# Kernel optimization log

Hardware: AMD Instinct MI355X
Metric: run time of the kernel (lower is better)

## Reference

```python
import jax, jax.numpy as jnp
import numpy as np

IN_DIM, HID, OUT_DIM = 2048, 2560, 2048
KERNEL = 4  # causal depthwise temporal conv width (Griffin uses 4)
C_RGLRU = 8.0  # Griffin's fixed scalar c in a_t = a^(c*r_t)


def setup_inputs() -> dict:
    key = jax.random.key(0)
    ks = jax.random.split(key, 16)
    s = 0.02
    return {
        "x": jax.random.normal(ks[0], (4, 2048, IN_DIM), jnp.float32),
        "Wl": jax.random.normal(ks[1], (IN_DIM, HID), jnp.float32) * s,
        "bl": jnp.zeros((HID,), jnp.float32),
        "Wr": jax.random.normal(ks[2], (IN_DIM, HID), jnp.float32) * s,
        "br": jnp.zeros((HID,), jnp.float32),
        "conv_w": jax.random.normal(ks[3], (KERNEL, 1, HID), jnp.float32) * 0.1,
        "conv_b": jnp.zeros((HID,), jnp.float32),
        "Wa": jax.random.normal(ks[4], (HID, HID), jnp.float32) * s,
        "ba": jnp.zeros((HID,), jnp.float32),
        "Wi": jax.random.normal(ks[5], (HID, HID), jnp.float32) * s,
        "bi": jnp.zeros((HID,), jnp.float32),
        "lam": jax.random.normal(ks[6], (HID,), jnp.float32) + 2.0,  # Lambda; sigmoid(lam)~0.88 decay
        "Wo": jax.random.normal(ks[7], (HID, OUT_DIM), jnp.float32) * s,
        "bo": jnp.zeros((OUT_DIM,), jnp.float32),
    }


def _rg_lru(u, Wa, ba, Wi, bi, lam):
    # u: [B,S,H]. a_t = exp(c * r_t * log sigmoid(lam)); log sigmoid = -softplus(-lam)
    r = jax.nn.sigmoid(jnp.einsum("bsh,hk->bsk", u, Wa) + ba)
    i = jax.nn.sigmoid(jnp.einsum("bsh,hk->bsk", u, Wi) + bi)
    log_a = (-C_RGLRU * jax.nn.softplus(-lam)) * r          # [B,S,H], <= 0
    a = jnp.exp(log_a)
    beta = jnp.sqrt(jnp.maximum(1.0 - jnp.exp(2.0 * log_a), 1e-12))
    drive = beta * (i * u)                                   # [B,S,H]

    def step(h, ab):
        a_t, d_t = ab
        h = a_t * h + d_t
        return h, h

    h0 = jnp.zeros((u.shape[0], u.shape[2]), u.dtype)
    _, hs = jax.lax.scan(step, h0, (a.transpose(1, 0, 2), drive.transpose(1, 0, 2)))
    return hs.transpose(1, 0, 2)  # [B,S,H]


def reference(x, Wl, bl, Wr, br, conv_w, conv_b, Wa, ba, Wi, bi, lam, Wo, bo):
    # left (GLU) branch
    left = jax.nn.gelu(jnp.einsum("bsd,dh->bsh", x, Wl) + bl)
    # right branch: linear -> causal depthwise conv1d -> RG-LRU
    r_in = jnp.einsum("bsd,dh->bsh", x, Wr) + br             # [B,S,H]
    conv = jax.lax.conv_general_dilated(
        r_in, conv_w, window_strides=(1,), padding=[(KERNEL - 1, 0)],
        dimension_numbers=("NWC", "WIO", "NWC"), feature_group_count=HID,
    ) + conv_b
    right = _rg_lru(conv, Wa, ba, Wi, bi, lam)
    return jnp.einsum("bsh,ho->bso", left * right, Wo) + bo
```

## Files before the change

kernel.cpp:

```cpp
#include <hip/hip_runtime.h>
#include <stdint.h>

#define B_ 4
#define S_ 2048
#define D_ 2048
#define H_ 2560
#define O_ 2048
#define M_ (B_*S_)
#define NCH 16
#define LCH (S_/NCH)

typedef __attribute__((ext_vector_type(8))) short bf16x8;
typedef __attribute__((ext_vector_type(4))) float f32x4;

typedef const __attribute__((address_space(1))) unsigned int* gp32;
typedef __attribute__((address_space(3))) unsigned int* lp32;

__device__ __forceinline__ void async_cp16(const unsigned short* g, unsigned short* l) {
    __builtin_amdgcn_global_load_lds((gp32)g, (lp32)l, 16, 0, 0);
}

__device__ __forceinline__ unsigned short f2bf(float f) {
    unsigned int x = __float_as_uint(f);
    x += 0x7fffu + ((x >> 16) & 1u);
    return (unsigned short)(x >> 16);
}
__device__ __forceinline__ float bf2f(unsigned short s) {
    return __uint_as_float(((unsigned int)s) << 16);
}
__device__ __forceinline__ float4 ld_bf4(const unsigned short* p) {
    const uint2 u = *(const uint2*)p;
    float4 r;
    r.x = bf2f((unsigned short)(u.x & 0xffffu));
    r.y = bf2f((unsigned short)(u.x >> 16));
    r.z = bf2f((unsigned short)(u.y & 0xffffu));
    r.w = bf2f((unsigned short)(u.y >> 16));
    return r;
}
__device__ __forceinline__ float fast_sigmoid(float x) { return 1.0f / (1.0f + __expf(-x)); }
__device__ __forceinline__ float gelu_tanh(float x) {
    float t = 0.7978845608028654f * (x + 0.044715f * x * x * x);
    float e = __expf(2.0f * t);
    float th = 1.0f - 2.0f / (e + 1.0f);
    return 0.5f * x * (1.0f + th);
}

__global__ void cast_x_kernel(const float* __restrict__ in, unsigned short* __restrict__ out, int n4) {
    int gid = blockIdx.x * 256 + threadIdx.x;
    if (gid >= n4) return;
    const float4 v = ((const float4*)in)[gid];
    union { unsigned short s[4]; uint2 u; } pk;
    pk.s[0] = f2bf(v.x); pk.s[1] = f2bf(v.y); pk.s[2] = f2bf(v.z); pk.s[3] = f2bf(v.w);
    ((uint2*)out)[gid] = pk.u;
}

__global__ void transpose_cast_kernel(const float* __restrict__ in, unsigned short* __restrict__ out,
                                      int K, int N) {
    __shared__ float tile[64][65];
    const int t = threadIdx.x;
    const int k0 = blockIdx.y * 64, n0 = blockIdx.x * 64;
    const int r = t >> 4, c4 = (t & 15) * 4;
    #pragma unroll
    for (int p = 0; p < 4; ++p) {
        const float4 v = *(const float4*)(in + (size_t)(k0 + p*16 + r) * N + n0 + c4);
        tile[p*16 + r][c4+0] = v.x;
        tile[p*16 + r][c4+1] = v.y;
        tile[p*16 + r][c4+2] = v.z;
        tile[p*16 + r][c4+3] = v.w;
    }
    __syncthreads();
    #pragma unroll
    for (int p = 0; p < 4; ++p) {
        const int nn = n0 + p*16 + r;
        union { unsigned short s[4]; uint2 u; } pk;
        #pragma unroll
        for (int j = 0; j < 4; ++j) pk.s[j] = f2bf(tile[c4 + j][p*16 + r]);
        *(uint2*)(out + (size_t)nn * K + k0 + c4) = pk.u;
    }
}

template <int MODE>
__global__ __launch_bounds__(256, 4) void gemm_kernel(
        const unsigned short* __restrict__ A,
        const unsigned short* __restrict__ Bt,
        const int K,
        const float* __restrict__ bias0,
        const float* __restrict__ bias1,
        void* __restrict__ out0,
        void* __restrict__ out1)
{
    __shared__ __align__(16) unsigned short As[128*64];
    __shared__ __align__(16) unsigned short Bs[128*64];
    const int t = threadIdx.x;
    const int m0 = blockIdx.y * 128;
    const int n0 = blockIdx.x * 128;

    const int srow = t >> 3;
    const int csrc = ((t & 7) ^ (srow & 7)) * 8;
    const unsigned short* gA = A  + (size_t)(m0 + srow) * K + csrc;
    const unsigned short* gB = Bt + (size_t)(n0 + srow) * K + csrc;
    unsigned short* lA = As + t * 8;
    unsigned short* lB = Bs + t * 8;
    const size_t gstep = (size_t)32 * K;

    const int lane = t & 63;
    const int w = t >> 6;
    const int wm = (w >> 1) * 64;
    const int wn = (w & 1) * 64;
    const int q = lane >> 4;
    const int l16 = lane & 15;

    f32x4 acc[4][4];
    #pragma unroll
    for (int i = 0; i < 4; ++i)
        #pragma unroll
        for (int j = 0; j < 4; ++j)
            acc[i][j] = (f32x4){0.f, 0.f, 0.f, 0.f};

    for (int k0 = 0; k0 < K; k0 += 64) {
        #pragma unroll
        for (int j = 0; j < 4; ++j) {
            async_cp16(gA + j * gstep, lA + j * 2048);
            async_cp16(gB + j * gstep, lB + j * 2048);
        }
        gA += 64; gB += 64;
        __syncthreads();
        #pragma unroll
        for (int ks = 0; ks < 2; ++ks) {
            const int ch = ((q + ks * 4) ^ (l16 & 7)) * 8;
            bf16x8 af[4], bfr[4];
            #pragma unroll
            for (int f = 0; f < 4; ++f)
                af[f]  = *(const bf16x8*)(As + (wm + f*16 + l16) * 64 + ch);
            #pragma unroll
            for (int f = 0; f < 4; ++f)
                bfr[f] = *(const bf16x8*)(Bs + (wn + f*16 + l16) * 64 + ch);
            #pragma unroll
            for (int fm = 0; fm < 4; ++fm)
                #pragma unroll
                for (int fn = 0; fn < 4; ++fn)
                    acc[fm][fn] = __builtin_amdgcn_mfma_f32_16x16x32_bf16(af[fm], bfr[fn], acc[fm][fn], 0, 0, 0);
        }
        __syncthreads();
    }

    const int rbase = q * 4;
    #pragma unroll
    for (int fm = 0; fm < 4; ++fm) {
        #pragma unroll
        for (int fn = 0; fn < 4; ++fn) {
            const int cc = n0 + wn + fn * 16 + l16;
            #pragma unroll
            for (int j = 0; j < 4; ++j) {
                const int rr = m0 + wm + fm * 16 + rbase + j;
                float v = acc[fm][fn][j];
                if (MODE == 0) {
                    if (cc < H_) {
                        ((unsigned short*)out0)[(size_t)rr * H_ + cc] = f2bf(gelu_tanh(v + bias0[cc]));
                    } else {
                        const int c2 = cc - H_;
                        ((unsigned short*)out1)[(size_t)rr * H_ + c2] = f2bf(v + bias1[c2]);
                    }
                } else if (MODE == 1) {
                    if (cc < H_) {
                        ((unsigned short*)out0)[(size_t)rr * H_ + cc] = f2bf(fast_sigmoid(v + bias0[cc]));
                    } else {
                        const int c2 = cc - H_;
                        ((unsigned short*)out1)[(size_t)rr * H_ + c2] = f2bf(fast_sigmoid(v + bias1[c2]));
                    }
                } else {
                    ((float*)out0)[(size_t)rr * O_ + cc] = v + bias0[cc];
                }
            }
        }
    }
}

__global__ void conv_kernel(const unsigned short* __restrict__ rin,
                            const float* __restrict__ cw,
                            const float* __restrict__ cb,
                            unsigned short* __restrict__ ub)
{
    const int gid = blockIdx.x * 256 + threadIdx.x;
    const int h = (gid % (H_/4)) * 4;
    const int tmp = gid / (H_/4);
    const int s0 = (tmp % (S_/4)) * 4;
    const int b = tmp / (S_/4);
    const unsigned short* base = rin + (size_t)b * S_ * H_ + h;
    float4 rows[7];
    #pragma unroll
    for (int idx = 0; idx < 7; ++idx) {
        const int s = s0 - 3 + idx;
        if (s >= 0) rows[idx] = ld_bf4(base + (size_t)s * H_);
        else        rows[idx] = make_float4(0.f, 0.f, 0.f, 0.f);
    }
    float4 w[4];
    #pragma unroll
    for (int j = 0; j < 4; ++j) w[j] = *(const float4*)(cw + j * H_ + h);
    const float4 bias = *(const float4*)(cb + h);
    #pragma unroll
    for (int p = 0; p < 4; ++p) {
        float ox = bias.x, oy = bias.y, oz = bias.z, ow = bias.w;
        #pragma unroll
        for (int j = 0; j < 4; ++j) {
            ox += w[j].x * rows[p + j].x;
            oy += w[j].y * rows[p + j].y;
            oz += w[j].z * rows[p + j].z;
            ow += w[j].w * rows[p + j].w;
        }
        const size_t oidx = (size_t)b * S_ * H_ + (size_t)(s0 + p) * H_ + h;
        union { unsigned short s4[4]; uint2 uu; } pk;
        pk.s4[0] = f2bf(ox); pk.s4[1] = f2bf(oy); pk.s4[2] = f2bf(oz); pk.s4[3] = f2bf(ow);
        *(uint2*)(ub + oidx) = pk.uu;
    }
}

__global__ void scan_pass1(const unsigned short* __restrict__ rg,
                           const unsigned short* __restrict__ ig,
                           const unsigned short* __restrict__ ub,
                           const float* __restrict__ lam,
                           float* __restrict__ Asum,
                           float* __restrict__ Hend)
{
    const int tid = blockIdx.x * 256 + threadIdx.x;
    const int h = tid % H_;
    const int t2 = tid / H_;
    const int c = t2 % NCH;
    const int b = t2 / NCH;
    const float kh = -8.0f * log1pf(__expf(-lam[h]));
    size_t idx = ((size_t)b * S_ + (size_t)c * LCH) * H_ + h;
    float A = 1.f, hs = 0.f;
    #pragma unroll 4
    for (int s = 0; s < LCH; ++s, idx += H_) {
        const float rv = bf2f(rg[idx]);
        const float iv = bf2f(ig[idx]);
        const float uv = bf2f(ub[idx]);
        const float a = __expf(kh * rv);
        const float beta = sqrtf(fmaxf(1.f - a * a, 1e-12f));
        hs = a * hs + beta * iv * uv;
        A *= a;
    }
    Asum[tid] = A;
    Hend[tid] = hs;
}

__global__ void scan_pass2(const float* __restrict__ Asum, float* __restrict__ Hend) {
    const int tid = blockIdx.x * 256 + threadIdx.x;
    const int h = tid % H_;
    const int b = tid / H_;
    float hin = 0.f;
    #pragma unroll
    for (int c = 0; c < NCH; ++c) {
        const int q = (b * NCH + c) * H_ + h;
        const float Ac = Asum[q];
        const float he = Hend[q];
        Hend[q] = hin;
        hin = he + Ac * hin;
    }
}

__global__ void scan_pass3(const unsigned short* __restrict__ rg,
                           const unsigned short* __restrict__ ig,
                           const unsigned short* __restrict__ ub,
                           const unsigned short* __restrict__ leftb,
                           const float* __restrict__ lam,
                           const float* __restrict__ Hin,
                           unsigned short* __restrict__ lrb)
{
    const int tid = blockIdx.x * 256 + threadIdx.x;
    const int h = tid % H_;
    const int t2 = tid / H_;
    const int c = t2 % NCH;
    const int b = t2 / NCH;
    const float kh = -8.0f * log1pf(__expf(-lam[h]));
    size_t idx = ((size_t)b * S_ + (size_t)c * LCH) * H_ + h;
    float hs = Hin[tid];
    #pragma unroll 4
    for (int s = 0; s < LCH; ++s, idx += H_) {
        const float rv = bf2f(rg[idx]);
        const float iv = bf2f(ig[idx]);
        const float uv = bf2f(ub[idx]);
        const float lf = bf2f(leftb[idx]);
        const float a = __expf(kh * rv);
        const float beta = sqrtf(fmaxf(1.f - a * a, 1e-12f));
        hs = a * hs + beta * iv * uv;
        lrb[idx] = f2bf(lf * hs);
    }
}

extern "C" void kernel_launch(void* const* d_in, const int* in_sizes, int n_in,
                              void* d_out, int out_size, void* d_ws, size_t ws_size,
                              hipStream_t stream)
{
    const float* x   = (const float*)d_in[0];
    const float* Wl  = (const float*)d_in[1];
    const float* bl  = (const float*)d_in[2];
    const float* Wr  = (const float*)d_in[3];
    const float* br  = (const float*)d_in[4];
    const float* cw  = (const float*)d_in[5];
    const float* cb  = (const float*)d_in[6];
    const float* Wa  = (const float*)d_in[7];
    const float* ba  = (const float*)d_in[8];
    const float* Wi  = (const float*)d_in[9];
    const float* bi  = (const float*)d_in[10];
    const float* lam = (const float*)d_in[11];
    const float* Wo  = (const float*)d_in[12];
    const float* bo  = (const float*)d_in[13];
    float* out = (float*)d_out;
    (void)in_sizes; (void)n_in; (void)out_size;

    const size_t wWlr = (size_t)2 * H_ * D_ * 2;
    const size_t wWai = (size_t)2 * H_ * H_ * 2;
    const size_t wWo  = (size_t)O_ * H_ * 2;
    auto al = [](size_t b) { return (b + 255) & ~(size_t)255; };

    int nchunk = 4;
    for (int n = 1; n <= 4; n *= 2) {
        const size_t Mc = M_ / n;
        const size_t Bc = Mc / S_;
        const size_t need = al(wWlr) + al(wWai) + al(wWo)
                          + 4 * al(Mc * H_ * 2)
                          + 2 * al(Bc * NCH * H_ * 4);
        if (need <= ws_size) { nchunk = n; break; }
    }
    const int Mc = M_ / nchunk;
    const int Bc = Mc / S_;
    const size_t actB = (size_t)Mc * H_ * 2;

    char* p = (char*)d_ws;
    size_t off = 0;
    auto alloc = [&](size_t bytes) -> void* {
        void* q = p + off;
        off += al(bytes);
        return q;
    };
    unsigned short* WlrT  = (unsigned short*)alloc(wWlr);
    unsigned short* WaiT  = (unsigned short*)alloc(wWai);
    unsigned short* WoT   = (unsigned short*)alloc(wWo);
    unsigned short* slotX = (unsigned short*)alloc(actB);
    unsigned short* slotL = (unsigned short*)alloc(actB);
    unsigned short* slotR = (unsigned short*)alloc(actB);
    unsigned short* slotU = (unsigned short*)alloc(actB);
    float* Asum = (float*)alloc((size_t)Bc * NCH * H_ * 4);
    float* Hend = (float*)alloc((size_t)Bc * NCH * H_ * 4);

    transpose_cast_kernel<<<dim3(H_/64, D_/64), dim3(256), 0, stream>>>(Wl, WlrT, D_, H_);
    transpose_cast_kernel<<<dim3(H_/64, D_/64), dim3(256), 0, stream>>>(Wr, WlrT + (size_t)H_*D_, D_, H_);
    transpose_cast_kernel<<<dim3(H_/64, H_/64), dim3(256), 0, stream>>>(Wa, WaiT, H_, H_);
    transpose_cast_kernel<<<dim3(H_/64, H_/64), dim3(256), 0, stream>>>(Wi, WaiT + (size_t)H_*H_, H_, H_);
    transpose_cast_kernel<<<dim3(O_/64, H_/64), dim3(256), 0, stream>>>(Wo, WoT, H_, O_);

    for (int c = 0; c < nchunk; ++c) {
        const float* xc = x + (size_t)c * Mc * D_;
        float* outc = out + (size_t)c * Mc * O_;
        unsigned short* xb    = slotX;
        unsigned short* leftb = slotL;
        unsigned short* rinb  = slotR;
        unsigned short* ub    = slotU;
        unsigned short* rgb   = slotX;
        unsigned short* igb   = slotR;
        unsigned short* lrb   = slotX;

        cast_x_kernel<<<dim3(Mc*D_/4/256), dim3(256), 0, stream>>>(xc, xb, Mc*D_/4);
        gemm_kernel<0><<<dim3((2*H_)/128, Mc/128), dim3(256), 0, stream>>>(xb, WlrT, D_, bl, br, leftb, rinb);
        conv_kernel<<<dim3(Bc*S_*H_/16/256), dim3(256), 0, stream>>>(rinb, cw, cb, ub);
        gemm_kernel<1><<<dim3((2*H_)/128, Mc/128), dim3(256), 0, stream>>>(ub, WaiT, H_, ba, bi, rgb, igb);
        scan_pass1<<<dim3(Bc*NCH*H_/256), dim3(256), 0, stream>>>(rgb, igb, ub, lam, Asum, Hend);
        scan_pass2<<<dim3(Bc*H_/256), dim3(256), 0, stream>>>(Asum, Hend);
        scan_pass3<<<dim3(Bc*NCH*H_/256), dim3(256), 0, stream>>>(rgb, igb, ub, leftb, lam, Hend, lrb);
        gemm_kernel<2><<<dim3(O_/128, Mc/128), dim3(256), 0, stream>>>(lrb, WoT, H_, bo, nullptr, outc, nullptr);
    }
}
```

Baseline: 811.2 us.

## Rewrite GEMM as 256x256 double-buffered ping-pong pipeline with grid swizzle

Replaces the single-buffered 128x128 GEMM with a 256x256 tile, 512-thread kernel that double-buffers A and B in LDS, issues async global-to-LDS loads for the next k-tile between quarter-steps of MFMA work, and uses explicit barriers, waitcnt and setprio to interleave loads with compute. It also remaps block indices with an XCD-style swizzle to improve L2 locality, and restructures the epilogue so left/right branch selection is per-block. This aims to hide global load latency and raise arithmetic intensity, at the cost of 128KB of LDS per block, more registers, and fragile hand-tuned synchronisation.

Result: slower. 848.8 us (+4.6%).

```diff
diff --git a/kernel.cpp b/kernel.cpp
--- a/kernel.cpp
+++ b/kernel.cpp
@@ -79,8 +79,106 @@
     }
 }
 
+#define GEMM_TILE(ASC, BSC, BSN, TT)                                           \
+  do {                                                                         \
+    const int kb_b = ((TT) + 1 < nt) ? ((TT) + 1) * 64 : 0;                    \
+    const int kb_a = ((TT) + 2 < nt) ? ((TT) + 2) * 64 : 0;                    \
+                \
+    _Pragma("unroll")                                                          \
+    for (int f = 0; f < 4; ++f) {                                              \
+      a0[f][0] = *(const bf16x8*)(ASC + rbaseA + f * 1024 + ch0);              \
+      a0[f][1] = *(const bf16x8*)(ASC + rbaseA + f * 1024 + ch1);              \
+    }                                                                          \
+    _Pragma("unroll")                                                          \
+    for (int f = 0; f < 2; ++f) {                                              \
+      b0[f][0] = *(const bf16x8*)(BSC + rbaseB + f * 1024 + ch0);              \
+      b0[f][1] = *(const bf16x8*)(BSC + rbaseB + f * 1024 + ch1);              \
+    }                                                                          \
+    async_cp16(gB + kb_b,          BSN + ldst);                                \
+    async_cp16(gB + kb_b + gr64,   BSN + ldst + 4096);                         \
+    __builtin_amdgcn_s_barrier();                                              \
+    asm volatile("s_waitcnt lgkmcnt(0)" ::: "memory");                         \
+    __builtin_amdgcn_sched_barrier(0);                                         \
+    __builtin_amdgcn_s_setprio(1);                                             \
+    _Pragma("unroll")                                                          \
+    for (int ks = 0; ks < 2; ++ks)                                             \
+      _Pragma("unroll")                                                        \
+      for (int f = 0; f < 4; ++f)                                              \
+        _Pragma("unroll")                                                      \
+        for (int g = 0; g < 2; ++g)                                            \
+          acc[f][g] = __builtin_amdgcn_mfma_f32_16x16x32_bf16(                 \
+              a0[f][ks], b0[g][ks], acc[f][g], 0, 0, 0);                       \
+    __builtin_amdgcn_s_setprio(0);                                             \
+    __builtin_amdgcn_s_barrier();                                              \
+    __builtin_amdgcn_sched_barrier(0);                                         \
+                   \
+    _Pragma("unroll")                                                          \
+    for (int f = 0; f < 4; ++f) {                                              \
+      a1[f][0] = *(const bf16x8*)(ASC + rbaseA + 4096 + f * 1024 + ch0);       \
+      a1[f][1] = *(const bf16x8*)(ASC + rbaseA + 4096 + f * 1024 + ch1);       \
+    }                                                                          \
+    async_cp16(gB + kb_b + 2 * gr64, BSN + 8192 + ldst);                       \
+    async_cp16(gB + kb_b + 3 * gr64, BSN + 8192 + ldst + 4096);                \
+    __builtin_amdgcn_s_barrier();                                              \
+    asm volatile("s_waitcnt lgkmcnt(0)" ::: "memory");                         \
+    __builtin_amdgcn_sched_barrier(0);                                         \
+    __builtin_amdgcn_s_setprio(1);                                             \
+    _Pragma("unroll")                                                          \
+    for (int ks = 0; ks < 2; ++ks)                                             \
+      _Pragma("unroll")                                                        \
+      for (int f = 0; f < 4; ++f)                                              \
+        _Pragma("unroll")                                                      \
+        for (int g = 0; g < 2; ++g)                                            \
+          acc[4 + f][g] = __builtin_amdgcn_mfma_f32_16x16x32_bf16(             \
+              a1[f][ks], b0[g][ks], acc[4 + f][g], 0, 0, 0);                   \
+    __builtin_amdgcn_s_setprio(0);                                             \
+    __builtin_amdgcn_s_barrier();                                              \
+    __builtin_amdgcn_sched_barrier(0);                                         \
+                   \
+    _Pragma("unroll")                                                          \
+    for (int f = 0; f < 2; ++f) {                                              \
+      b1[f][0] = *(const bf16x8*)(BSC + rbaseB + 2048 + f * 1024 + ch0);       \
+      b1[f][1] = *(const bf16x8*)(BSC + rbaseB + 2048 + f * 1024 + ch1);       \
+    }                                                                          \
+    async_cp16(gA + kb_a,        ASC + ldst);                                  \
+    async_cp16(gA + kb_a + gr64, ASC + ldst + 4096);                           \
+    __builtin_amdgcn_s_barrier();                                              \
+    asm volatile("s_waitcnt lgkmcnt(0)" ::: "memory");                         \
+    __builtin_amdgcn_sched_barrier(0);                                         \
+    __builtin_amdgcn_s_setprio(1);                                             \
+    _Pragma("unroll")                                                          \
+    for (int ks = 0; ks < 2; ++ks)                                             \
+      _Pragma("unroll")                                                        \
+      for (int f = 0; f < 4; ++f)                                              \
+        _Pragma("unroll")                                                      \
+        for (int g = 0; g < 2; ++g)                                            \
+          acc[f][2 + g] = __builtin_amdgcn_mfma_f32_16x16x32_bf16(             \
+              a0[f][ks], b1[g][ks], acc[f][2 + g], 0, 0, 0);                   \
+    __builtin_amdgcn_s_setprio(0);                                             \
+    __builtin_amdgcn_s_barrier();                                              \
+    __builtin_amdgcn_sched_barrier(0);                                         \
+                  \
+    async_cp16(gA + kb_a + 2 * gr64, ASC + 8192 + ldst);                       \
+    async_cp16(gA + kb_a + 3 * gr64, ASC + 8192 + ldst + 4096);                \
+    asm volatile("s_waitcnt vmcnt(4)" ::: "memory");                           \
+    __builtin_amdgcn_sched_barrier(0);                                         \
+    __builtin_amdgcn_s_barrier();                                              \
+    __builtin_amdgcn_s_setprio(1);                                             \
+    _Pragma("unroll")                                                          \
+    for (int ks = 0; ks < 2; ++ks)                                             \
+      _Pragma("unroll")                                                        \
+      for (int f = 0; f < 4; ++f)                                              \
+        _Pragma("unroll")                                                      \
+        for (int g = 0; g < 2; ++g)                                            \
+          acc[4 + f][2 + g] = __builtin_amdgcn_mfma_f32_16x16x32_bf16(         \
+              a1[f][ks], b1[g][ks], acc[4 + f][2 + g], 0, 0, 0);               \
+    __builtin_amdgcn_s_setprio(0);                                             \
+    __builtin_amdgcn_s_barrier();                                              \
+    __builtin_amdgcn_sched_barrier(0);                                         \
+  } while (0)
+
 template <int MODE>
-__global__ __launch_bounds__(256, 4) void gemm_kernel(
+__global__ __launch_bounds__(512, 2) void gemm_kernel(
         const unsigned short* __restrict__ A,
         const unsigned short* __restrict__ Bt,
         const int K,
@@ -89,87 +187,105 @@
         void* __restrict__ out0,
         void* __restrict__ out1)
 {
-    __shared__ __align__(16) unsigned short As[128*64];
-    __shared__ __align__(16) unsigned short Bs[128*64];
+    __shared__ __align__(16) unsigned short As0[256*64];
+    __shared__ __align__(16) unsigned short As1[256*64];
+    __shared__ __align__(16) unsigned short Bs0[256*64];
+    __shared__ __align__(16) unsigned short Bs1[256*64];
+
     const int t = threadIdx.x;
-    const int m0 = blockIdx.y * 128;
-    const int n0 = blockIdx.x * 128;
+
+    const int nx = gridDim.x;
+    const int nwg = gridDim.x * gridDim.y;
+    int lin = blockIdx.y * nx + blockIdx.x;
+    lin = (lin & 7) * (nwg >> 3) + (lin >> 3);
+    const int m0 = (lin / nx) * 256;
+    const int n0 = (lin % nx) * 256;
 
     const int srow = t >> 3;
-    const int csrc = ((t & 7) ^ (srow & 7)) * 8;
-    const unsigned short* gA = A  + (size_t)(m0 + srow) * K + csrc;
-    const unsigned short* gB = Bt + (size_t)(n0 + srow) * K + csrc;
-    unsigned short* lA = As + t * 8;
-    unsigned short* lB = Bs + t * 8;
-    const size_t gstep = (size_t)32 * K;
+    const int scol = ((t & 7) ^ (srow & 7)) * 8;
+    const unsigned short* gA = A  + (size_t)(m0 + srow) * K + scol;
+    const unsigned short* gB = Bt + (size_t)(n0 + srow) * K + scol;
+    const size_t gr64 = (size_t)64 * K;
+    const int ldst = t * 8;
 
     const int lane = t & 63;
     const int w = t >> 6;
-    const int wm = (w >> 1) * 64;
-    const int wn = (w & 1) * 64;
+    const int wm = w >> 2;
+    const int wn = w & 3;
     const int q = lane >> 4;
     const int l16 = lane & 15;
 
-    f32x4 acc[4][4];
-    #pragma unroll
-    for (int i = 0; i < 4; ++i)
+    const int rbaseA = (wm * 128 + l16) * 64;
+    const int rbaseB = (wn * 64 + l16) * 64;
+    const int ch0 = ((q)     ^ (l16 & 7)) * 8;
+    const int ch1 = ((q + 4) ^ (l16 & 7)) * 8;
+
+    const int nt = K >> 6;
+
+    f32x4 acc[8][4];
+    #pragma unroll
+    for (int i = 0; i < 8; ++i)
         #pragma unroll
         for (int j = 0; j < 4; ++j)
             acc[i][j] = (f32x4){0.f, 0.f, 0.f, 0.f};
 
-    for (int k0 = 0; k0 < K; k0 += 64) {
+    bf16x8 a0[4][2], a1[4][2], b0[2][2], b1[2][2];
+
+    async_cp16(gA,            As0 + ldst);
+    async_cp16(gA + gr64,     As0 + ldst + 4096);
+    async_cp16(gA + 2*gr64,   As0 + 8192 + ldst);
+    async_cp16(gA + 3*gr64,   As0 + 8192 + ldst + 4096);
+    async_cp16(gB,            Bs0 + ldst);
+    async_cp16(gB + gr64,     Bs0 + ldst + 4096);
+    async_cp16(gB + 2*gr64,   Bs0 + 8192 + ldst);
+    async_cp16(gB + 3*gr64,   Bs0 + 8192 + ldst + 4096);
+    async_cp16(gA + 64,           As1 + ldst);
+    async_cp16(gA + 64 + gr64,    As1 + ldst + 4096);
+    async_cp16(gA + 64 + 2*gr64,  As1 + 8192 + ldst);
+    async_cp16(gA + 64 + 3*gr64,  As1 + 8192 + ldst + 4096);
+    asm volatile("s_waitcnt vmcnt(4)" ::: "memory");
+    __builtin_amdgcn_sched_barrier(0);
+    __builtin_amdgcn_s_barrier();
+
+    for (int tt = 0; tt < nt; tt += 2) {
+        GEMM_TILE(As0, Bs0, Bs1, tt);
+        GEMM_TILE(As1, Bs1, Bs0, tt + 1);
+    }
+    asm volatile("s_waitcnt vmcnt(0)" ::: "memory");
+
+    const int rb = q * 4;
+    if (MODE == 2) {
+        float* op = (float*)out0;
         #pragma unroll
-        for (int j = 0; j < 4; ++j) {
-            async_cp16(gA + j * gstep, lA + j * 2048);
-            async_cp16(gB + j * gstep, lB + j * 2048);
-        }
-        gA += 64; gB += 64;
-        __syncthreads();
-        #pragma unroll
-        for (int ks = 0; ks < 2; ++ks) {
-            const int ch = ((q + ks * 4) ^ (l16 & 7)) * 8;
-            bf16x8 af[4], bfr[4];
-            #pragma unroll
-            for (int f = 0; f < 4; ++f)
-                af[f]  = *(const bf16x8*)(As + (wm + f*16 + l16) * 64 + ch);
-            #pragma unroll
-            for (int f = 0; f < 4; ++f)
-                bfr[f] = *(const bf16x8*)(Bs + (wn + f*16 + l16) * 64 + ch);
-            #pragma unroll
-            for (int fm = 0; fm < 4; ++fm)
-                #pragma unroll
-                for (int fn = 0; fn < 4; ++fn)
-                    acc[fm][fn] = __builtin_amdgcn_mfma_f32_16x16x32_bf16(af[fm], bfr[fn], acc[fm][fn], 0, 0, 0);
-        }
-        __syncthreads();
-    }
-
-    const int rbase = q * 4;
-    #pragma unroll
-    for (int fm = 0; fm < 4; ++fm) {
-        #pragma unroll
-        for (int fn = 0; fn < 4; ++fn) {
-            const int cc = n0 + wn + fn * 16 + l16;
+        for (int i = 0; i < 8; ++i) {
+            const int rr = m0 + wm * 128 + (i >> 2) * 64 + (i & 3) * 16 + rb;
             #pragma unroll
             for (int j = 0; j < 4; ++j) {
-                const int rr = m0 + wm + fm * 16 + rbase + j;
-                float v = acc[fm][fn][j];
-                if (MODE == 0) {
-                    if (cc < H_) {
-                        ((unsigned short*)out0)[(size_t)rr * H_ + cc] = f2bf(gelu_tanh(v + bias0[cc]));
-                    } else {
-                        const int c2 = cc - H_;
-                        ((unsigned short*)out1)[(size_t)rr * H_ + c2] = f2bf(v + bias1[c2]);
-                    }
-                } else if (MODE == 1) {
-                    if (cc < H_) {
-                        ((unsigned short*)out0)[(size_t)rr * H_ + cc] = f2bf(fast_sigmoid(v + bias0[cc]));
-                    } else {
-                        const int c2 = cc - H_;
-                        ((unsigned short*)out1)[(size_t)rr * H_ + c2] = f2bf(fast_sigmoid(v + bias1[c2]));
-                    }
-                } else {
-                    ((float*)out0)[(size_t)rr * O_ + cc] = v + bias0[cc];
+                const int cc = n0 + wn * 64 + (j >> 1) * 32 + (j & 1) * 16 + l16;
+                const float bb = bias0[cc];
+                #pragma unroll
+                for (int jj = 0; jj < 4; ++jj)
+                    op[(size_t)(rr + jj) * O_ + cc] = acc[i][j][jj] + bb;
+            }
+        }
+    } else {
+        const bool left = (n0 < H_);
+        const float* bias = left ? bias0 : bias1;
+        unsigned short* op = (unsigned short*)(left ? out0 : out1);
+        const int nb = left ? n0 : (n0 - H_);
+        #pragma unroll
+        for (int i = 0; i < 8; ++i) {
+            const int rr = m0 + wm * 128 + (i >> 2) * 64 + (i & 3) * 16 + rb;
+            #pragma unroll
+            for (int j = 0; j < 4; ++j) {
+                const int cc = nb + wn * 64 + (j >> 1) * 32 + (j & 1) * 16 + l16;
+                const float bb = bias[cc];
+                #pragma unroll
+                for (int jj = 0; jj < 4; ++jj) {
+                    float v = acc[i][j][jj] + bb;
+                    if (MODE == 0) v = left ? gelu_tanh(v) : v;
+                    else           v = fast_sigmoid(v);
+                    op[(size_t)(rr + jj) * H_ + cc] = f2bf(v);
                 }
             }
         }
@@ -362,12 +478,12 @@
         unsigned short* lrb   = slotX;
 
         cast_x_kernel<<<dim3(Mc*D_/4/256), dim3(256), 0, stream>>>(xc, xb, Mc*D_/4);
-        gemm_kernel<0><<<dim3((2*H_)/128, Mc/128), dim3(256), 0, stream>>>(xb, WlrT, D_, bl, br, leftb, rinb);
+        gemm_kernel<0><<<dim3((2*H_)/256, Mc/256), dim3(512), 0, stream>>>(xb, WlrT, D_, bl, br, leftb, rinb);
         conv_kernel<<<dim3(Bc*S_*H_/16/256), dim3(256), 0, stream>>>(rinb, cw, cb, ub);
-        gemm_kernel<1><<<dim3((2*H_)/128, Mc/128), dim3(256), 0, stream>>>(ub, WaiT, H_, ba, bi, rgb, igb);
+        gemm_kernel<1><<<dim3((2*H_)/256, Mc/256), dim3(512), 0, stream>>>(ub, WaiT, H_, ba, bi, rgb, igb);
         scan_pass1<<<dim3(Bc*NCH*H_/256), dim3(256), 0, stream>>>(rgb, igb, ub, lam, Asum, Hend);
         scan_pass2<<<dim3(Bc*H_/256), dim3(256), 0, stream>>>(Asum, Hend);
         scan_pass3<<<dim3(Bc*NCH*H_/256), dim3(256), 0, stream>>>(rgb, igb, ub, leftb, lam, Hend, lrb);
-        gemm_kernel<2><<<dim3(O_/128, Mc/128), dim3(256), 0, stream>>>(lrb, WoT, H_, bo, nullptr, outc, nullptr);
-    }
-}
+        gemm_kernel<2><<<dim3(O_/256, Mc/256), dim3(512), 0, stream>>>(lrb, WoT, H_, bo, nullptr, outc, nullptr);
+    }
+}
```

## Use 256x256-tile ping-pong pipelined GEMM for output projection

Applied to the files above, without the earlier changes.

Replaces the 128x128 output-projection GEMM with a new 512-thread kernel using 256x256 tiles, double-buffered LDS with async global-to-LDS copies, interleaved partial-tile MFMA phases with priority hints, and a grouped block-index remap for L2 locality. The aim is more data reuse per loaded tile and overlap of loads with MFMA work. It uses 128KB of LDS per block and a large accumulator set, which constrains occupancy, and the grid of 8x(Mc/256) blocks may underfill the device for small chunks.

New measurement: 835.2 us. 1.03x slower.

```diff
diff --git a/kernel.cpp b/kernel.cpp
--- a/kernel.cpp
+++ b/kernel.cpp
@@ -172,6 +172,149 @@
                     ((float*)out0)[(size_t)rr * O_ + cc] = v + bias0[cc];
                 }
             }
+        }
+    }
+}
+
+#define LDA2(dst, base)                                                        \
+    _Pragma("unroll")                                                          \
+    for (int f = 0; f < 4; ++f) {                                              \
+      dst[f][0] = *(const bf16x8*)((base) + rbaseA + f * 1024 + ch0);          \
+      dst[f][1] = *(const bf16x8*)((base) + rbaseA + f * 1024 + ch1);          \
+    }
+#define LDB2(dst, base)                                                        \
+    _Pragma("unroll")                                                          \
+    for (int f = 0; f < 2; ++f) {                                              \
+      dst[f][0] = *(const bf16x8*)((base) + rbaseB + f * 1024 + ch0);          \
+      dst[f][1] = *(const bf16x8*)((base) + rbaseB + f * 1024 + ch1);          \
+    }
+#define MM2(ar, br, i0, j0)                                                    \
+    __builtin_amdgcn_s_setprio(1);                                             \
+    _Pragma("unroll")                                                          \
+    for (int ks = 0; ks < 2; ++ks)                                             \
+      _Pragma("unroll")                                                        \
+      for (int f = 0; f < 4; ++f)                                              \
+        _Pragma("unroll")                                                      \
+        for (int g = 0; g < 2; ++g)                                            \
+          acc[(i0) + f][(j0) + g] = __builtin_amdgcn_mfma_f32_16x16x32_bf16(   \
+              ar[f][ks], br[g][ks], acc[(i0) + f][(j0) + g], 0, 0, 0);         \
+    __builtin_amdgcn_s_setprio(0);
+#define STG2(gptr, kk, lbuf, half)                                             \
+    async_cp16((gptr) + (size_t)(kk) + (size_t)((half)*2)   * gr64,            \
+               (lbuf) + (half)*8192 + ldst);                                   \
+    async_cp16((gptr) + (size_t)(kk) + (size_t)((half)*2+1) * gr64,            \
+               (lbuf) + (half)*8192 + ldst + 4096);
+#define BAR2() __builtin_amdgcn_s_barrier()
+
+__global__ __launch_bounds__(512, 2) void gemm256_k2(
+        const unsigned short* __restrict__ A,
+        const unsigned short* __restrict__ Bt,
+        const int K,
+        const float* __restrict__ bias0,
+        float* __restrict__ out0)
+{
+    __shared__ __align__(16) unsigned short As0[256*64];
+    __shared__ __align__(16) unsigned short As1[256*64];
+    __shared__ __align__(16) unsigned short Bs0[256*64];
+    __shared__ __align__(16) unsigned short Bs1[256*64];
+
+    const int t = threadIdx.x;
+
+    const int nx = gridDim.x;
+    const int nwg = gridDim.x * gridDim.y;
+    int lin = blockIdx.y * nx + blockIdx.x;
+    lin = (lin & 7) * (nwg >> 3) + (lin >> 3);
+    const int m0 = (lin / nx) * 256;
+    const int n0 = (lin % nx) * 256;
+
+    const int srow = t >> 3;
+    const int scol = ((t & 7) ^ (srow & 7)) * 8;
+    const unsigned short* gA = A  + (size_t)(m0 + srow) * K + scol;
+    const unsigned short* gB = Bt + (size_t)(n0 + srow) * K + scol;
+    const size_t gr64 = (size_t)64 * K;
+    const int ldst = t * 8;
+
+    const int lane = t & 63;
+    const int w = t >> 6;
+    const int wm = w >> 2;
+    const int wn = w & 3;
+    const int q = lane >> 4;
+    const int l16 = lane & 15;
+
+    const int rbaseA = (wm * 128 + l16) * 64;
+    const int rbaseB = (wn * 64 + l16) * 64;
+    const int ch0 = ((q)     ^ (l16 & 7)) * 8;
+    const int ch1 = ((q + 4) ^ (l16 & 7)) * 8;
+
+    const int nt = K >> 6;
+
+    f32x4 acc[8][4];
+    #pragma unroll
+    for (int i = 0; i < 8; ++i)
+        #pragma unroll
+        for (int j = 0; j < 4; ++j)
+            acc[i][j] = (f32x4){0.f, 0.f, 0.f, 0.f};
+
+    bf16x8 a0[4][2], a1[4][2], b0[2][2], b1[2][2];
+
+    STG2(gA, 0, As0, 0); STG2(gA, 0, As0, 1);
+    STG2(gB, 0, Bs0, 0); STG2(gB, 0, Bs0, 1);
+    STG2(gA, 64, As1, 0); STG2(gA, 64, As1, 1);
+    asm volatile("s_waitcnt vmcnt(4)" ::: "memory");
+    BAR2();
+
+    for (int tt = 0; tt < nt; tt += 2) {
+        const size_t kb1 = (size_t)((tt + 1 < nt) ? (tt + 1) * 64 : 0);
+        const size_t ka2 = (size_t)((tt + 2 < nt) ? (tt + 2) * 64 : 0);
+        const size_t kb2 = ka2;
+        const size_t ka3 = (size_t)((tt + 3 < nt) ? (tt + 3) * 64 : 0);
+
+        LDA2(a0, As0); LDB2(b0, Bs0);
+        STG2(gB, kb1, Bs1, 0);
+        MM2(a0, b0, 0, 0);
+        BAR2();
+        LDA2(a1, As0 + 4096);
+        STG2(gB, kb1, Bs1, 1);
+        MM2(a1, b0, 4, 0);
+        BAR2();
+        LDB2(b1, Bs0 + 2048);
+        STG2(gA, ka2, As0, 0);
+        MM2(a0, b1, 0, 2);
+        BAR2();
+        STG2(gA, ka2, As0, 1);
+        MM2(a1, b1, 4, 2);
+        asm volatile("s_waitcnt vmcnt(4)" ::: "memory");
+        BAR2();
+        LDA2(a0, As1); LDB2(b0, Bs1);
+        STG2(gB, kb2, Bs0, 0);
+        MM2(a0, b0, 0, 0);
+        BAR2();
+        LDA2(a1, As1 + 4096);
+        STG2(gB, kb2, Bs0, 1);
+        MM2(a1, b0, 4, 0);
+        BAR2();
+        LDB2(b1, Bs1 + 2048);
+        STG2(gA, ka3, As1, 0);
+        MM2(a0, b1, 0, 2);
+        BAR2();
+        STG2(gA, ka3, As1, 1);
+        MM2(a1, b1, 4, 2);
+        asm volatile("s_waitcnt vmcnt(4)" ::: "memory");
+        BAR2();
+    }
+    asm volatile("s_waitcnt vmcnt(0)" ::: "memory");
+
+    const int rb = q * 4;
+    #pragma unroll
+    for (int i = 0; i < 8; ++i) {
+        const int rr = m0 + wm * 128 + (i >> 2) * 64 + (i & 3) * 16 + rb;
+        #pragma unroll
+        for (int j = 0; j < 4; ++j) {
+            const int cc = n0 + wn * 64 + (j >> 1) * 32 + (j & 1) * 16 + l16;
+            const float bb = bias0[cc];
+            #pragma unroll
+            for (int jj = 0; jj < 4; ++jj)
+                out0[(size_t)(rr + jj) * O_ + cc] = acc[i][j][jj] + bb;
         }
     }
 }
@@ -368,6 +511,6 @@
         scan_pass1<<<dim3(Bc*NCH*H_/256), dim3(256), 0, stream>>>(rgb, igb, ub, lam, Asum, Hend);
         scan_pass2<<<dim3(Bc*H_/256), dim3(256), 0, stream>>>(Asum, Hend);
         scan_pass3<<<dim3(Bc*NCH*H_/256), dim3(256), 0, stream>>>(rgb, igb, ub, leftb, lam, Hend, lrb);
-        gemm_kernel<2><<<dim3(O_/128, Mc/128), dim3(256), 0, stream>>>(lrb, WoT, H_, bo, nullptr, outc, nullptr);
-    }
-}
+        gemm256_k2<<<dim3(O_/256, Mc/256), dim3(512), 0, stream>>>(lrb, WoT, H_, bo, outc);
+    }
+}
```

## Vectorize scan passes to 4 channels per thread, raise chunk count, merge weight transposes

Applied to the files above, without the earlier changes.

Each scan thread now handles four adjacent hidden channels, using 8-byte bf16 loads and stores instead of 2-byte scalar accesses. The sequence chunk count rises from 16 to 64, which keeps the number of scan threads up while shortening each serial chunk. The five weight transpose-cast launches become one launch with a z-dimension selecting the matrix. The goal is better memory coalescing and fewer launches, at the cost of more partial-sum traffic and a longer serial pass2.

Measured after the change: 850.2 us, median of 2. +4.8%, slower.

```diff
diff --git a/kernel.cpp b/kernel.cpp
--- a/kernel.cpp
+++ b/kernel.cpp
@@ -7,7 +7,7 @@
 #define H_ 2560
 #define O_ 2048
 #define M_ (B_*S_)
-#define NCH 16
+#define NCH 64
 #define LCH (S_/NCH)
 
 typedef __attribute__((ext_vector_type(8))) short bf16x8;
@@ -37,6 +37,11 @@
     r.w = bf2f((unsigned short)(u.y >> 16));
     return r;
 }
+__device__ __forceinline__ uint2 st_bf4(float a, float b, float c, float d) {
+    union { unsigned short s[4]; uint2 u; } pk;
+    pk.s[0] = f2bf(a); pk.s[1] = f2bf(b); pk.s[2] = f2bf(c); pk.s[3] = f2bf(d);
+    return pk.u;
+}
 __device__ __forceinline__ float fast_sigmoid(float x) { return 1.0f / (1.0f + __expf(-x)); }
 __device__ __forceinline__ float gelu_tanh(float x) {
     float t = 0.7978845608028654f * (x + 0.044715f * x * x * x);
@@ -49,20 +54,31 @@
     int gid = blockIdx.x * 256 + threadIdx.x;
     if (gid >= n4) return;
     const float4 v = ((const float4*)in)[gid];
-    union { unsigned short s[4]; uint2 u; } pk;
-    pk.s[0] = f2bf(v.x); pk.s[1] = f2bf(v.y); pk.s[2] = f2bf(v.z); pk.s[3] = f2bf(v.w);
-    ((uint2*)out)[gid] = pk.u;
-}
-
-__global__ void transpose_cast_kernel(const float* __restrict__ in, unsigned short* __restrict__ out,
-                                      int K, int N) {
+    ((uint2*)out)[gid] = st_bf4(v.x, v.y, v.z, v.w);
+}
+
+__global__ void transpose_all_kernel(const float* __restrict__ Wl, const float* __restrict__ Wr,
+                                     const float* __restrict__ Wa, const float* __restrict__ Wi,
+                                     const float* __restrict__ Wo,
+                                     unsigned short* __restrict__ WlrT,
+                                     unsigned short* __restrict__ WaiT,
+                                     unsigned short* __restrict__ WoT) {
     __shared__ float tile[64][65];
+    const float* src; unsigned short* dst; int K, N;
+    switch (blockIdx.z) {
+        case 0:  src = Wl; dst = WlrT;                       K = D_; N = H_; break;
+        case 1:  src = Wr; dst = WlrT + (size_t)H_ * D_;     K = D_; N = H_; break;
+        case 2:  src = Wa; dst = WaiT;                       K = H_; N = H_; break;
+        case 3:  src = Wi; dst = WaiT + (size_t)H_ * H_;     K = H_; N = H_; break;
+        default: src = Wo; dst = WoT;                        K = H_; N = O_; break;
+    }
+    const int k0 = blockIdx.y * 64, n0 = blockIdx.x * 64;
+    if (k0 >= K || n0 >= N) return;
     const int t = threadIdx.x;
-    const int k0 = blockIdx.y * 64, n0 = blockIdx.x * 64;
     const int r = t >> 4, c4 = (t & 15) * 4;
     #pragma unroll
     for (int p = 0; p < 4; ++p) {
-        const float4 v = *(const float4*)(in + (size_t)(k0 + p*16 + r) * N + n0 + c4);
+        const float4 v = *(const float4*)(src + (size_t)(k0 + p*16 + r) * N + n0 + c4);
         tile[p*16 + r][c4+0] = v.x;
         tile[p*16 + r][c4+1] = v.y;
         tile[p*16 + r][c4+2] = v.z;
@@ -72,10 +88,9 @@
     #pragma unroll
     for (int p = 0; p < 4; ++p) {
         const int nn = n0 + p*16 + r;
-        union { unsigned short s[4]; uint2 u; } pk;
-        #pragma unroll
-        for (int j = 0; j < 4; ++j) pk.s[j] = f2bf(tile[c4 + j][p*16 + r]);
-        *(uint2*)(out + (size_t)nn * K + k0 + c4) = pk.u;
+        *(uint2*)(dst + (size_t)nn * K + k0 + c4) =
+            st_bf4(tile[c4+0][p*16 + r], tile[c4+1][p*16 + r],
+                   tile[c4+2][p*16 + r], tile[c4+3][p*16 + r]);
     }
 }
 
@@ -209,9 +224,7 @@
             ow += w[j].w * rows[p + j].w;
         }
         const size_t oidx = (size_t)b * S_ * H_ + (size_t)(s0 + p) * H_ + h;
-        union { unsigned short s4[4]; uint2 uu; } pk;
-        pk.s4[0] = f2bf(ox); pk.s4[1] = f2bf(oy); pk.s4[2] = f2bf(oz); pk.s4[3] = f2bf(ow);
-        *(uint2*)(ub + oidx) = pk.uu;
+        *(uint2*)(ub + oidx) = st_bf4(ox, oy, oz, ow);
     }
 }
 
@@ -223,39 +236,56 @@
                            float* __restrict__ Hend)
 {
     const int tid = blockIdx.x * 256 + threadIdx.x;
-    const int h = tid % H_;
-    const int t2 = tid / H_;
+    const int h4 = (tid % (H_/4)) * 4;
+    const int t2 = tid / (H_/4);
     const int c = t2 % NCH;
     const int b = t2 / NCH;
-    const float kh = -8.0f * log1pf(__expf(-lam[h]));
-    size_t idx = ((size_t)b * S_ + (size_t)c * LCH) * H_ + h;
-    float A = 1.f, hs = 0.f;
+    const float4 lm = *(const float4*)(lam + h4);
+    float kh[4];
+    kh[0] = -8.0f * log1pf(__expf(-lm.x));
+    kh[1] = -8.0f * log1pf(__expf(-lm.y));
+    kh[2] = -8.0f * log1pf(__expf(-lm.z));
+    kh[3] = -8.0f * log1pf(__expf(-lm.w));
+    size_t idx = ((size_t)b * S_ + (size_t)c * LCH) * H_ + h4;
+    float A[4] = {1.f, 1.f, 1.f, 1.f};
+    float hs[4] = {0.f, 0.f, 0.f, 0.f};
     #pragma unroll 4
     for (int s = 0; s < LCH; ++s, idx += H_) {
-        const float rv = bf2f(rg[idx]);
-        const float iv = bf2f(ig[idx]);
-        const float uv = bf2f(ub[idx]);
-        const float a = __expf(kh * rv);
-        const float beta = sqrtf(fmaxf(1.f - a * a, 1e-12f));
-        hs = a * hs + beta * iv * uv;
-        A *= a;
-    }
-    Asum[tid] = A;
-    Hend[tid] = hs;
-}
-
-__global__ void scan_pass2(const float* __restrict__ Asum, float* __restrict__ Hend) {
+        const float4 rv = ld_bf4(rg + idx);
+        const float4 iv = ld_bf4(ig + idx);
+        const float4 uv = ld_bf4(ub + idx);
+        const float rr[4] = {rv.x, rv.y, rv.z, rv.w};
+        const float ii[4] = {iv.x, iv.y, iv.z, iv.w};
+        const float uu[4] = {uv.x, uv.y, uv.z, uv.w};
+        #pragma unroll
+        for (int j = 0; j < 4; ++j) {
+            const float a = __expf(kh[j] * rr[j]);
+            const float beta = sqrtf(fmaxf(1.f - a * a, 1e-12f));
+            hs[j] = a * hs[j] + beta * ii[j] * uu[j];
+            A[j] *= a;
+        }
+    }
+    const size_t o = ((size_t)b * NCH + c) * H_ + h4;
+    *(float4*)(Asum + o) = make_float4(A[0], A[1], A[2], A[3]);
+    *(float4*)(Hend + o) = make_float4(hs[0], hs[1], hs[2], hs[3]);
+}
+
+__global__ void scan_pass2(const float* __restrict__ Asum, float* __restrict__ Hend, int n) {
     const int tid = blockIdx.x * 256 + threadIdx.x;
-    const int h = tid % H_;
-    const int b = tid / H_;
-    float hin = 0.f;
-    #pragma unroll
+    if (tid >= n) return;
+    const int h4 = (tid % (H_/4)) * 4;
+    const int b = tid / (H_/4);
+    float4 hin = make_float4(0.f, 0.f, 0.f, 0.f);
+    #pragma unroll 8
     for (int c = 0; c < NCH; ++c) {
-        const int q = (b * NCH + c) * H_ + h;
-        const float Ac = Asum[q];
-        const float he = Hend[q];
-        Hend[q] = hin;
-        hin = he + Ac * hin;
+        const size_t q = ((size_t)b * NCH + c) * H_ + h4;
+        const float4 Ac = *(const float4*)(Asum + q);
+        const float4 he = *(const float4*)(Hend + q);
+        *(float4*)(Hend + q) = hin;
+        hin.x = he.x + Ac.x * hin.x;
+        hin.y = he.y + Ac.y * hin.y;
+        hin.z = he.z + Ac.z * hin.z;
+        hin.w = he.w + Ac.w * hin.w;
     }
 }
 
@@ -268,23 +298,39 @@
                            unsigned short* __restrict__ lrb)
 {
     const int tid = blockIdx.x * 256 + threadIdx.x;
-    const int h = tid % H_;
-    const int t2 = tid / H_;
+    const int h4 = (tid % (H_/4)) * 4;
+    const int t2 = tid / (H_/4);
     const int c = t2 % NCH;
     const int b = t2 / NCH;
-    const float kh = -8.0f * log1pf(__expf(-lam[h]));
-    size_t idx = ((size_t)b * S_ + (size_t)c * LCH) * H_ + h;
-    float hs = Hin[tid];
+    const float4 lm = *(const float4*)(lam + h4);
+    float kh[4];
+    kh[0] = -8.0f * log1pf(__expf(-lm.x));
+    kh[1] = -8.0f * log1pf(__expf(-lm.y));
+    kh[2] = -8.0f * log1pf(__expf(-lm.z));
+    kh[3] = -8.0f * log1pf(__expf(-lm.w));
+    size_t idx = ((size_t)b * S_ + (size_t)c * LCH) * H_ + h4;
+    const size_t o = ((size_t)b * NCH + c) * H_ + h4;
+    const float4 h0 = *(const float4*)(Hin + o);
+    float hs[4] = {h0.x, h0.y, h0.z, h0.w};
     #pragma unroll 4
     for (int s = 0; s < LCH; ++s, idx += H_) {
-        const float rv = bf2f(rg[idx]);
-        const float iv = bf2f(ig[idx]);
-        const float uv = bf2f(ub[idx]);
-        const float lf = bf2f(leftb[idx]);
-        const float a = __expf(kh * rv);
-        const float beta = sqrtf(fmaxf(1.f - a * a, 1e-12f));
-        hs = a * hs + beta * iv * uv;
-        lrb[idx] = f2bf(lf * hs);
+        const float4 rv = ld_bf4(rg + idx);
+        const float4 iv = ld_bf4(ig + idx);
+        const float4 uv = ld_bf4(ub + idx);
+        const float4 lf = ld_bf4(leftb + idx);
+        const float rr[4] = {rv.x, rv.y, rv.z, rv.w};
+        const float ii[4] = {iv.x, iv.y, iv.z, iv.w};
+        const float uu[4] = {uv.x, uv.y, uv.z, uv.w};
+        const float ll[4] = {lf.x, lf.y, lf.z, lf.w};
+        float lr[4];
+        #pragma unroll
+        for (int j = 0; j < 4; ++j) {
+            const float a = __expf(kh[j] * rr[j]);
+            const float beta = sqrtf(fmaxf(1.f - a * a, 1e-12f));
+            hs[j] = a * hs[j] + beta * ii[j] * uu[j];
+            lr[j] = ll[j] * hs[j];
+        }
+        *(uint2*)(lrb + idx) = st_bf4(lr[0], lr[1], lr[2], lr[3]);
     }
 }
 
@@ -344,11 +390,8 @@
     float* Asum = (float*)alloc((size_t)Bc * NCH * H_ * 4);
     float* Hend = (float*)alloc((size_t)Bc * NCH * H_ * 4);
 
-    transpose_cast_kernel<<<dim3(H_/64, D_/64), dim3(256), 0, stream>>>(Wl, WlrT, D_, H_);
-    transpose_cast_kernel<<<dim3(H_/64, D_/64), dim3(256), 0, stream>>>(Wr, WlrT + (size_t)H_*D_, D_, H_);
-    transpose_cast_kernel<<<dim3(H_/64, H_/64), dim3(256), 0, stream>>>(Wa, WaiT, H_, H_);
-    transpose_cast_kernel<<<dim3(H_/64, H_/64), dim3(256), 0, stream>>>(Wi, WaiT + (size_t)H_*H_, H_, H_);
-    transpose_cast_kernel<<<dim3(O_/64, H_/64), dim3(256), 0, stream>>>(Wo, WoT, H_, O_);
+    transpose_all_kernel<<<dim3(40, 40, 5), dim3(256), 0, stream>>>(
+        Wl, Wr, Wa, Wi, Wo, WlrT, WaiT, WoT);
 
     for (int c = 0; c < nchunk; ++c) {
         const float* xc = x + (size_t)c * Mc * D_;
@@ -365,9 +408,12 @@
         gemm_kernel<0><<<dim3((2*H_)/128, Mc/128), dim3(256), 0, stream>>>(xb, WlrT, D_, bl, br, leftb, rinb);
         conv_kernel<<<dim3(Bc*S_*H_/16/256), dim3(256), 0, stream>>>(rinb, cw, cb, ub);
         gemm_kernel<1><<<dim3((2*H_)/128, Mc/128), dim3(256), 0, stream>>>(ub, WaiT, H_, ba, bi, rgb, igb);
-        scan_pass1<<<dim3(Bc*NCH*H_/256), dim3(256), 0, stream>>>(rgb, igb, ub, lam, Asum, Hend);
-        scan_pass2<<<dim3(Bc*H_/256), dim3(256), 0, stream>>>(Asum, Hend);
-        scan_pass3<<<dim3(Bc*NCH*H_/256), dim3(256), 0, stream>>>(rgb, igb, ub, leftb, lam, Hend, lrb);
+        scan_pass1<<<dim3(Bc*NCH*(H_/4)/256), dim3(256), 0, stream>>>(rgb, igb, ub, lam, Asum, Hend);
+        {
+            const int n2 = Bc * (H_/4);
+            scan_pass2<<<dim3((n2 + 255)/256), dim3(256), 0, stream>>>(Asum, Hend, n2);
+        }
+        scan_pass3<<<dim3(Bc*NCH*(H_/4)/256), dim3(256), 0, stream>>>(rgb, igb, ub, leftb, lam, Hend, lrb);
         gemm_kernel<2><<<dim3(O_/128, Mc/128), dim3(256), 0, stream>>>(lrb, WoT, H_, bo, nullptr, outc, nullptr);
     }
 }
```
